# Optimization experiments

Measured on AMD Instinct MI355X. Metric: run time of the kernel, lower is better.

## Reference

```python
import jax, jax.numpy as jnp
import numpy as np

M, N, T = 4, 48, 256
H1 = (M + N) * 80          # 4160, linear1 out / GRU input
HID = M * M + N * N        # 2320, GRU hidden
H2 = M * N * 4             # 768
OUT = M * N                # 192


def _w(k, shape, fan_in):
    return jax.random.normal(k, shape, jnp.float32) / np.float32(np.sqrt(fan_in))


def setup_inputs() -> dict:
    key = jax.random.key(0)
    ks = jax.random.split(key, 12)
    A = (0.95 * jnp.eye(M, dtype=jnp.float32)
         + 0.05 * jax.random.normal(ks[0], (M, M), jnp.float32))  # stable dynamics
    return {
        "y_seq": jax.random.normal(ks[1], (N, T), jnp.float32),
        "x0": jax.random.normal(ks[2], (M,), jnp.float32),
        "h0": jax.random.normal(ks[3], (HID,), jnp.float32),  # self.hn (randn, zero_hidden_state=False)
        "A": A,
        "C": _w(ks[4], (N, M + 1), M + 1),
        "W1": _w(ks[5], (H1, M + N), M + N),
        "b1": jnp.zeros((H1,), jnp.float32),
        "W_ih": _w(ks[6], (3 * HID, H1), H1),
        "W_hh": _w(ks[7], (3 * HID, HID), HID),
        "b_ih": jnp.zeros((3 * HID,), jnp.float32),
        "b_hh": jnp.zeros((3 * HID,), jnp.float32),
        "W2": _w(ks[8], (H2, HID), HID),
        "b2": jnp.zeros((H2,), jnp.float32),
        "W3": _w(ks[9], (OUT, H2), H2),
        "b3": jnp.zeros((OUT,), jnp.float32),
    }


def _l2n(v):
    # torch F.normalize(p=2, eps=1e-12)
    return v / jnp.maximum(jnp.linalg.norm(v), 1e-12)


def reference(y_seq, x0, h0, A, C, W1, b1, W_ih, W_hh, b_ih, b_hh, W2, b2, W3, b3):
    m, n = A.shape[0], C.shape[0]
    one = jnp.ones((1,), A.dtype)

    def step(carry, y):
        x_post, h = carry
        x_prior = A @ x_post                                   # [m]
        y_prior = C @ jnp.concatenate([x_prior, one])           # [n]
        f2 = _l2n(y - y_prior)
        f4 = _l2n(x_post - x_prior)
        kg_in = jnp.concatenate([f2, f4])                       # [n+m]
        l1 = jax.nn.relu(W1 @ kg_in + b1)                       # [H1]
        # single GRU step (torch gate order: r, z, n)
        gi = W_ih @ l1 + b_ih
        gh = W_hh @ h + b_hh
        ir, iz, ig = jnp.split(gi, 3)
        hr, hz, hg = jnp.split(gh, 3)
        r = jax.nn.sigmoid(ir + hr)
        z = jax.nn.sigmoid(iz + hz)
        g = jnp.tanh(ig + r * hg)
        h_new = (1.0 - z) * g + z * h                           # [HID]
        l2 = jax.nn.relu(W2 @ h_new + b2)                       # [H2]
        kg = ((W3 @ l2 + b3) / 10000.0).reshape(m, n)           # Kalman gain
        x_new = x_prior + kg @ (y - y_prior)                    # posterior
        return (x_new, h_new), x_new

    _, xs = jax.lax.scan(step, (x0, h0), y_seq.T)               # xs: [T, m]
    return xs.T                                                 # [m, T]
```

## Files before the change

kernel.cpp:

```cpp
#include <hip/hip_runtime.h>
#include <hip/hip_cooperative_groups.h>

namespace cg = cooperative_groups;

#define T_STEPS 256

#define O_SLOT  0
#define O_EPOCH 1024
#define O_ZP    2048
#define O_HF    6144
#define HF_STR  9280
#define O_HB    24704
#define HB_STR  4672
#define O_GI    34048
#define O_GH    61888
#define O_PIH   90112
#define O_PHH   57997312
#define O_W2B   90514432
#define NEED_MIN 94077952
#define O_W1P   94077952
#define NEED_FULL 94543872

#define N_W2  1781760

#define WS_L1  0
#define WS_H0  4160
#define WS_H1  6480
#define WS_L2  8800
#define WS_V   9568
#define WS_C   12640

typedef __attribute__((ext_vector_type(8))) short bf16x8;
typedef __attribute__((ext_vector_type(4))) float f32x4;

__device__ __forceinline__ float wred(float v) {
#pragma unroll
  for (int m = 32; m; m >>= 1) v += __shfl_xor(v, m, 64);
  return v;
}
__device__ __forceinline__ float dot4(float4 a, float4 b) {
  return a.x * b.x + a.y * b.y + a.z * b.z + a.w * b.w;
}
__device__ __forceinline__ float blo(unsigned u) {
  unsigned t = u << 16; return __builtin_bit_cast(float, t);
}
__device__ __forceinline__ float bhi(unsigned u) {
  unsigned t = u & 0xFFFF0000u; return __builtin_bit_cast(float, t);
}
__device__ __forceinline__ float dot8bb(uint4 w, uint4 x) {
  float s;
  s  = blo(w.x) * blo(x.x) + bhi(w.x) * bhi(x.x);
  s += blo(w.y) * blo(x.y) + bhi(w.y) * bhi(x.y);
  s += blo(w.z) * blo(x.z) + bhi(w.z) * bhi(x.z);
  s += blo(w.w) * blo(x.w) + bhi(w.w) * bhi(x.w);
  return s;
}
__device__ __forceinline__ unsigned short f2bf(float f) {
  unsigned u = __builtin_bit_cast(unsigned, f);
  unsigned r = u + 0x7FFF + ((u >> 16) & 1);
  return (unsigned short)(r >> 16);
}

__device__ __forceinline__ void st_ag_f32(float* p, float v) {
  __hip_atomic_store(p, v, __ATOMIC_RELAXED, __HIP_MEMORY_SCOPE_AGENT);
}
__device__ __forceinline__ float ld_ag_f32(const float* p) {
  return __hip_atomic_load(p, __ATOMIC_RELAXED, __HIP_MEMORY_SCOPE_AGENT);
}
__device__ __forceinline__ void st_ag_u32(unsigned* p, unsigned v) {
  __hip_atomic_store(p, v, __ATOMIC_RELAXED, __HIP_MEMORY_SCOPE_AGENT);
}
__device__ __forceinline__ unsigned long long ld_ag_u64(const unsigned long long* p) {
  return __hip_atomic_load(p, __ATOMIC_RELAXED, __HIP_MEMORY_SCOPE_AGENT);
}

__device__ __forceinline__ void gbar(char* wsb, int bid, unsigned target, int* s_ok) {
  unsigned* slot  = (unsigned*)(wsb + O_SLOT);
  unsigned* epoch = (unsigned*)(wsb + O_EPOCH);
  const int tid = threadIdx.x;
  __syncthreads();
  if (bid == 0) {
    for (;;) {
      if (tid == 0) *s_ok = 1;
      __syncthreads();
      if (tid >= 1 && tid < 256) {
        if (__hip_atomic_load(&slot[tid], __ATOMIC_RELAXED, __HIP_MEMORY_SCOPE_AGENT) < target)
          *s_ok = 0;
      }
      __syncthreads();
      if (*s_ok) break;
      __builtin_amdgcn_s_sleep(2);
    }
    if (tid == 0)
      __hip_atomic_store(epoch, target, __ATOMIC_RELEASE, __HIP_MEMORY_SCOPE_AGENT);
    __syncthreads();
  } else {
    if (tid == 0) {
      __hip_atomic_store(&slot[bid], target, __ATOMIC_RELEASE, __HIP_MEMORY_SCOPE_AGENT);
      while (__hip_atomic_load(epoch, __ATOMIC_RELAXED, __HIP_MEMORY_SCOPE_AGENT) < target)
        __builtin_amdgcn_s_sleep(1);
    }
    __syncthreads();
  }
}

__global__ __launch_bounds__(256) void k_pack(const float* __restrict__ W,
                                              uint4* __restrict__ dst,
                                              int K, int NKT, int n) {
  int idx = blockIdx.x * 256 + threadIdx.x;
  int stride = gridDim.x * 256;
  for (; idx < n; idx += stride) {
    int l = idx & 63;
    int u = idx >> 6;
    int kt = u % NKT;
    int job = u / NKT;
    int g = job / 145, jt = job - g * 145;
    int row = g * 2320 + jt * 16 + (l & 15);
    int col = kt * 32 + ((l >> 4) << 3);
    const float* src = W + (size_t)row * K + col;
    unsigned short o[8];
    if (col + 7 < K) {
#pragma unroll
      for (int i = 0; i < 8; i++) o[i] = f2bf(src[i]);
    } else {
#pragma unroll
      for (int i = 0; i < 8; i++) o[i] = (col + i < K) ? f2bf(src[i]) : (unsigned short)0;
    }
    uint4 v;
    v.x = (unsigned)o[0] | ((unsigned)o[1] << 16);
    v.y = (unsigned)o[2] | ((unsigned)o[3] << 16);
    v.z = (unsigned)o[4] | ((unsigned)o[5] << 16);
    v.w = (unsigned)o[6] | ((unsigned)o[7] << 16);
    dst[idx] = v;
  }
}
__global__ __launch_bounds__(256) void k_cvt(const float4* __restrict__ src,
                                             ushort4* __restrict__ dst, int n4) {
  int i = blockIdx.x * 256 + threadIdx.x, st = gridDim.x * 256;
  for (; i < n4; i += st) {
    float4 v = src[i];
    ushort4 o;
    o.x = f2bf(v.x); o.y = f2bf(v.y); o.z = f2bf(v.z); o.w = f2bf(v.w);
    dst[i] = o;
  }
}
__global__ __launch_bounds__(256) void k_cvtw1(const float* __restrict__ W1,
                                               unsigned short* __restrict__ dst) {
  int i = blockIdx.x * 256 + threadIdx.x;
  if (i < 4160 * 56) {
    int r = i / 56, c = i - r * 56;
    dst[i] = (c < 52) ? f2bf(W1[r * 52 + c]) : (unsigned short)0;
  }
}
__global__ __launch_bounds__(256) void k_h0(const float* __restrict__ h0,
                                            unsigned short* __restrict__ hb0,
                                            unsigned short* __restrict__ hb1) {
  int j = blockIdx.x * 256 + threadIdx.x;
  if (j < 2336) {
    hb1[j] = (j < 2320) ? f2bf(h0[j]) : (unsigned short)0;
    if (j >= 2320) hb0[j] = 0;
  }
}

__global__ __launch_bounds__(1024, 4) void knet2(
    const float* __restrict__ y_seq, const float* __restrict__ x0,
    const float* __restrict__ h0, const float* __restrict__ A,
    const float* __restrict__ Cm, const float* __restrict__ W1,
    const float* __restrict__ b1, const float* __restrict__ b_ih,
    const float* __restrict__ b_hh, const float* __restrict__ b2,
    const float* __restrict__ W3, const float* __restrict__ b3,
    float* __restrict__ out, char* __restrict__ wsb, int use_w1p)
{
  const int tid  = threadIdx.x;
  const int lane = tid & 63;
  const int wav  = tid >> 6;
  const int bid  = blockIdx.x;

  float* zp  = (float*)(wsb + O_ZP);
  float* gi  = (float*)(wsb + O_GI);
  float* gh  = (float*)(wsb + O_GH);
  const unsigned short* bw2 = (const unsigned short*)(wsb + O_W2B);
  const uint4* w1p = (const uint4*)(wsb + O_W1P);

  __shared__ __align__(16) uint4 s_l1u[520];
  __shared__ __align__(16) uint4 s_h4u[292];
  __shared__ __align__(16) unsigned short s_h2[2336];
  __shared__ float s_part[4][4][16];
  __shared__ __align__(16) unsigned short s_kgb[64];
  __shared__ __align__(16) float s_kgf[52];
  __shared__ float s_innov[48];
  __shared__ float s_a[192];
  __shared__ float s_zred[384];
  __shared__ float s_l2loc[8];
  __shared__ float s_xpost[4], s_xprior[4], s_dx[4];
  __shared__ float s_sc2, s_sc4;
  __shared__ int s_ok;

  unsigned ep = 0;

  for (int t = 0; t <= T_STEPS; ++t) {
    if (t == 0) {
      if (tid < 4) s_xpost[tid] = x0[tid];
    } else {
      if (tid < 384) s_zred[tid] = ld_ag_f32(&zp[tid]);
      __syncthreads();
      if (tid < 4) {
        float z = 0.f;
#pragma unroll 8
        for (int p = 0; p < 96; ++p) z += s_zred[p * 4 + tid];
        float cb = 0.f;
        for (int j = 0; j < 48; ++j) cb += s_innov[j] * b3[tid * 48 + j];
        float xn = s_xprior[tid] + (z + cb) * 1e-4f;
        s_xpost[tid] = xn;
        if (bid == 0) out[tid * T_STEPS + (t - 1)] = xn;
      }
    }
    __syncthreads();
    if (t == T_STEPS) return;

    if (tid < 4) {
      float xpr = 0.f;
#pragma unroll
      for (int j = 0; j < 4; j++) xpr += A[tid * 4 + j] * s_xpost[j];
      s_xprior[tid] = xpr;
    }
    __syncthreads();
    if (tid < 48) {
      float yp = Cm[tid * 5 + 4];
#pragma unroll
      for (int j = 0; j < 4; j++) yp += Cm[tid * 5 + j] * s_xprior[j];
      s_innov[tid] = y_seq[tid * T_STEPS + t] - yp;
    }
    if (tid >= 64 && tid < 68) {
      int i = tid - 64;
      s_dx[i] = s_xpost[i] - s_xprior[i];
    }
    __syncthreads();
    if (tid == 0) {
      float s2 = 0.f;
      for (int r = 0; r < 48; r++) s2 += s_innov[r] * s_innov[r];
      s_sc2 = 1.0f / fmaxf(sqrtf(s2), 1e-12f);
      float s4 = 0.f;
      for (int i = 0; i < 4; i++) s4 += s_dx[i] * s_dx[i];
      s_sc4 = 1.0f / fmaxf(sqrtf(s4), 1e-12f);
    }
    __syncthreads();
    if (tid < 64) {
      float v = (tid < 48) ? s_innov[tid] * s_sc2
              : (tid < 52) ? s_dx[tid - 48] * s_sc4 : 0.f;
      s_kgb[tid] = f2bf(v);
      if (tid < 52) s_kgf[tid] = v;
    }
    {
      const unsigned long long* hbg =
          (const unsigned long long*)(wsb + O_HB + ((t + 1) & 1) * HB_STR);
      unsigned long long* dst = (unsigned long long*)s_h4u;
      if (tid < 584) dst[tid] = ld_ag_u64(hbg + tid);
    }
    __syncthreads();

    if (use_w1p) {
      const uint4* kg4 = (const uint4*)s_kgb;
      for (int r = tid; r < 4160; r += 1024) {
        const uint4* wr = w1p + (size_t)r * 7;
        float acc = b1[r];
#pragma unroll
        for (int c = 0; c < 7; c++) acc += dot8bb(wr[c], kg4[c]);
        ((unsigned short*)s_l1u)[r] = f2bf(fmaxf(acc, 0.f));
      }
    } else {
      const float4* kg4 = (const float4*)s_kgf;
      for (int r = tid; r < 4160; r += 1024) {
        const float4* wr = (const float4*)(W1 + (size_t)r * 52);
        float acc = b1[r];
#pragma unroll
        for (int c = 0; c < 13; c++) acc += dot4(wr[c], kg4[c]);
        ((unsigned short*)s_l1u)[r] = f2bf(fmaxf(acc, 0.f));
      }
    }
    __syncthreads();

    {
      const int q  = wav >> 2;
      const int kw = wav & 3;
      const int job = bid + 256 * q;
      if (job < 870) {
        const int side = (job < 435) ? 0 : 1;
        const int xoff = lane >> 4;
        const uint4* xs;
        const uint4* wp;
        int kbeg, kend;
        if (side == 0) {
          xs = s_l1u;
          kbeg = kw * 33; kend = kbeg + 33; if (kend > 130) kend = 130;
          wp = (const uint4*)(wsb + O_PIH) + ((size_t)job * 130 + kbeg) * 64 + lane;
        } else {
          xs = s_h4u;
          kbeg = kw * 19; kend = kbeg + 19; if (kend > 73) kend = 73;
          wp = (const uint4*)(wsb + O_PHH) + ((size_t)(job - 435) * 73 + kbeg) * 64 + lane;
        }
        f32x4 acc = {0.f, 0.f, 0.f, 0.f};
        uint4 b0  = wp[0 * 64];
        uint4 b1r = wp[1 * 64];
        uint4 b2r = wp[2 * 64];
        uint4 b3r = wp[3 * 64];
        uint4 b4  = wp[4 * 64];
        uint4 b5  = wp[5 * 64];
        uint4 b6  = wp[6 * 64];
        uint4 b7  = wp[7 * 64];
        int kt = kbeg;
#define GSTEP(P, B) { acc = __builtin_amdgcn_mfma_f32_16x16x32_bf16( \
            __builtin_bit_cast(bf16x8, B), \
            __builtin_bit_cast(bf16x8, xs[(kt + P) * 4 + xoff]), acc, 0, 0, 0); \
            B = wp[(size_t)(kt - kbeg + 8 + P) * 64]; }
        while (kt + 8 <= kend) {
          GSTEP(0, b0) GSTEP(1, b1r) GSTEP(2, b2r) GSTEP(3, b3r)
          GSTEP(4, b4) GSTEP(5, b5)  GSTEP(6, b6)  GSTEP(7, b7)
          kt += 8;
        }
#undef GSTEP
#define TSTEP(P, B) if (kt + P < kend) acc = __builtin_amdgcn_mfma_f32_16x16x32_bf16( \
            __builtin_bit_cast(bf16x8, B), \
            __builtin_bit_cast(bf16x8, xs[(kt + P) * 4 + xoff]), acc, 0, 0, 0);
        TSTEP(0, b0) TSTEP(1, b1r) TSTEP(2, b2r) TSTEP(3, b3r)
        TSTEP(4, b4) TSTEP(5, b5)  TSTEP(6, b6)  TSTEP(7, b7)
#undef TSTEP
        if ((lane & 15) == 0) {
          int rb = (lane >> 4) * 4;
#pragma unroll
          for (int i = 0; i < 4; i++) s_part[q][kw][rb + i] = acc[i];
        }
      }
    }
    __syncthreads();
    if (tid < 64) {
      int q = tid >> 4, r = tid & 15;
      int job = bid + 256 * q;
      if (job < 870) {
        float s = s_part[q][0][r] + s_part[q][1][r] + s_part[q][2][r] + s_part[q][3][r];
        if (job < 435) st_ag_f32(&gi[job * 16 + r], s);
        else st_ag_f32(&gh[(job - 435) * 16 + r], s);
      }
    }
    ++ep; gbar(wsb, bid, ep, &s_ok);

    if (bid < 96) {
      float* hf_out = (float*)(wsb + O_HF + (t & 1) * HF_STR);
      unsigned* hb_out32 = (unsigned*)(wsb + O_HB + (t & 1) * HB_STR);
      const float* hf_old = (const float*)(wsb + O_HF + ((t + 1) & 1) * HF_STR);
      for (int j = tid; j < 2320; j += 1024) {
        float ir = ld_ag_f32(&gi[j]) + b_ih[j];
        float iz = ld_ag_f32(&gi[2320 + j]) + b_ih[2320 + j];
        float ig = ld_ag_f32(&gi[4640 + j]) + b_ih[4640 + j];
        float hr = ld_ag_f32(&gh[j]) + b_hh[j];
        float hz = ld_ag_f32(&gh[2320 + j]) + b_hh[2320 + j];
        float hg = ld_ag_f32(&gh[4640 + j]) + b_hh[4640 + j];
        float rr = 1.f / (1.f + expf(-(ir + hr)));
        float zz = 1.f / (1.f + expf(-(iz + hz)));
        float gg = tanhf(ig + rr * hg);
        float hold = (t == 0) ? h0[j] : ld_ag_f32(&hf_old[j]);
        float hn = (1.f - zz) * gg + zz * hold;
        s_h2[j] = f2bf(hn);
        if (bid == 0) st_ag_f32(&hf_out[j], hn);
      }
      if (tid < 16) s_h2[2320 + tid] = 0;
      __syncthreads();
      if (bid == 0 && tid < 1168) {
        unsigned v = (unsigned)s_h2[2 * tid] | ((unsigned)s_h2[2 * tid + 1] << 16);
        st_ag_u32(hb_out32 + tid, v);
      }
      if (wav < 8) {
        const int row = bid * 8 + wav;
        const uint4* wr = (const uint4*)(bw2 + (size_t)row * 2320);
        const uint4* hx = (const uint4*)s_h2;
        float acc = 0.f;
        for (int k = lane; k < 290; k += 64) acc += dot8bb(wr[k], hx[k]);
        acc = wred(acc);
        if (lane == 0) s_l2loc[wav] = fmaxf(acc + b2[row], 0.f);
      }
      __syncthreads();
      if (tid < 192) {
        const float* w3r = W3 + (size_t)tid * 768 + bid * 8;
        float a = 0.f;
#pragma unroll
        for (int r = 0; r < 8; r++) a += w3r[r] * s_l2loc[r];
        s_a[tid] = a * s_innov[tid % 48];
      }
      __syncthreads();
      if (tid < 4) {
        float zv = 0.f;
        for (int j = 0; j < 48; j++) zv += s_a[tid * 48 + j];
        st_ag_f32(&zp[bid * 4 + tid], zv);
      }
    }
    ++ep; gbar(wsb, bid, ep, &s_ok);
  }
}

__global__ __launch_bounds__(256, 2) void knet(
    const float* __restrict__ y_seq, const float* __restrict__ x0,
    const float* __restrict__ h0, const float* __restrict__ A,
    const float* __restrict__ Cm, const float* __restrict__ W1,
    const float* __restrict__ b1, const float* __restrict__ W_ih,
    const float* __restrict__ W_hh, const float* __restrict__ b_ih,
    const float* __restrict__ b_hh, const float* __restrict__ W2,
    const float* __restrict__ b2, const float* __restrict__ W3,
    const float* __restrict__ b3, float* __restrict__ out,
    float* __restrict__ ws)
{
  cg::grid_group grid = cg::this_grid();
  const int tid = threadIdx.x, lane = tid & 63, wav = tid >> 6, bid = blockIdx.x;
  const int gt = bid * 256 + tid, wave_g = bid * 4 + wav, NW = gridDim.x * 4;

  __shared__ __align__(16) float4 s_buf4[1040];
  __shared__ __align__(16) float4 s_h4[580];
  __shared__ __align__(16) float s_kgin[52];
  __shared__ float s_innov[48];
  __shared__ float s_xpost[4], s_xprior[4], s_dx[4];
  __shared__ float s_sc2, s_sc4;

  for (int t = 0; t <= T_STEPS; ++t) {
    if (t == 0) {
      if (tid < 4) s_xpost[tid] = x0[tid];
    } else {
      const float4* vv  = (const float4*)(ws + WS_V + wav * 768);
      const float4* l2v = (const float4*)(ws + WS_L2);
      float acc = 0.f;
      for (int k = lane; k < 192; k += 64) acc += dot4(vv[k], l2v[k]);
      acc = wred(acc);
      if (lane == 0)
        s_xpost[wav] = s_xprior[wav] + (acc + ws[WS_C + wav]) * 1e-4f;
    }
    __syncthreads();
    if (bid == 0 && t > 0 && tid < 4) out[tid * T_STEPS + (t - 1)] = s_xpost[tid];
    if (t == T_STEPS) return;

    if (tid < 4) {
      float xp = 0.f;
#pragma unroll
      for (int j = 0; j < 4; j++) xp += A[tid * 4 + j] * s_xpost[j];
      s_xprior[tid] = xp;
    }
    __syncthreads();
    if (tid < 48) {
      float yp = Cm[tid * 5 + 4];
#pragma unroll
      for (int j = 0; j < 4; j++) yp += Cm[tid * 5 + j] * s_xprior[j];
      s_innov[tid] = y_seq[tid * T_STEPS + t] - yp;
    }
    if (tid >= 64 && tid < 68) {
      int i = tid - 64;
      s_dx[i] = s_xpost[i] - s_xprior[i];
    }
    __syncthreads();
    if (tid == 0) {
      float s2 = 0.f;
      for (int r = 0; r < 48; r++) s2 += s_innov[r] * s_innov[r];
      s_sc2 = 1.0f / fmaxf(sqrtf(s2), 1e-12f);
      float s4 = 0.f;
      for (int i = 0; i < 4; i++) s4 += s_dx[i] * s_dx[i];
      s_sc4 = 1.0f / fmaxf(sqrtf(s4), 1e-12f);
    }
    __syncthreads();
    if (tid < 48) s_kgin[tid] = s_innov[tid] * s_sc2;
    else if (tid < 52) s_kgin[tid] = s_dx[tid - 48] * s_sc4;
    __syncthreads();

    if (gt < 4160) {
      const float4* wr  = (const float4*)(W1 + (size_t)gt * 52);
      const float4* kg4 = (const float4*)s_kgin;
      float acc = b1[gt];
#pragma unroll
      for (int k = 0; k < 13; k++) acc += dot4(wr[k], kg4[k]);
      ws[WS_L1 + gt] = fmaxf(acc, 0.f);
    }
    grid.sync();

    {
      const float* h_old = (t == 0) ? h0 : (ws + (((t & 1) == 0) ? WS_H0 : WS_H1));
      float* h_new = ws + (((t & 1) == 0) ? WS_H1 : WS_H0);
      const float4* l1g = (const float4*)(ws + WS_L1);
      for (int i = tid; i < 1040; i += 256) s_buf4[i] = l1g[i];
      const float4* hog = (const float4*)h_old;
      for (int i = tid; i < 580; i += 256) s_h4[i] = hog[i];
      __syncthreads();
      const float* s_h = (const float*)s_h4;

      for (int j = wave_g; j < 2320; j += NW) {
        const float4* r0 = (const float4*)(W_ih + (size_t)j * 4160);
        const float4* r1 = (const float4*)(W_ih + (size_t)(j + 2320) * 4160);
        const float4* r2 = (const float4*)(W_ih + (size_t)(j + 4640) * 4160);
        float a0 = 0.f, a1 = 0.f, a2 = 0.f;
#pragma unroll 4
        for (int k = lane; k < 1040; k += 64) {
          float4 x = s_buf4[k];
          a0 += dot4(r0[k], x); a1 += dot4(r1[k], x); a2 += dot4(r2[k], x);
        }
        const float4* q0 = (const float4*)(W_hh + (size_t)j * 2320);
        const float4* q1 = (const float4*)(W_hh + (size_t)(j + 2320) * 2320);
        const float4* q2 = (const float4*)(W_hh + (size_t)(j + 4640) * 2320);
        float c0 = 0.f, c1 = 0.f, c2 = 0.f;
#pragma unroll 4
        for (int k = lane; k < 580; k += 64) {
          float4 x = s_h4[k];
          c0 += dot4(q0[k], x); c1 += dot4(q1[k], x); c2 += dot4(q2[k], x);
        }
        a0 = wred(a0); a1 = wred(a1); a2 = wred(a2);
        c0 = wred(c0); c1 = wred(c1); c2 = wred(c2);
        if (lane == 0) {
          float ir = a0 + b_ih[j], iz = a1 + b_ih[j + 2320], ig = a2 + b_ih[j + 4640];
          float hr = c0 + b_hh[j], hz = c1 + b_hh[j + 2320], hg = c2 + b_hh[j + 4640];
          float rr = 1.f / (1.f + expf(-(ir + hr)));
          float zz = 1.f / (1.f + expf(-(iz + hz)));
          float gg = tanhf(ig + rr * hg);
          h_new[j] = (1.f - zz) * gg + zz * s_h[j];
        }
      }
    }
    grid.sync();

    {
      const float* h_new = ws + (((t & 1) == 0) ? WS_H1 : WS_H0);
      const float4* hv = (const float4*)h_new;
      for (int i = tid; i < 580; i += 256) s_buf4[i] = hv[i];
      __syncthreads();

      if (gt < 3072) {
        int i = gt / 768, cc = gt - i * 768;
        const float* wcol = W3 + (size_t)(i * 48) * 768 + cc;
        float acc = 0.f;
#pragma unroll 8
        for (int j = 0; j < 48; j++) acc += s_innov[j] * wcol[(size_t)j * 768];
        ws[WS_V + gt] = acc;
      } else if (gt < 3076) {
        int i = gt - 3072;
        float acc = 0.f;
        for (int j = 0; j < 48; j++) acc += s_innov[j] * b3[i * 48 + j];
        ws[WS_C + i] = acc;
      }

      for (int task = wave_g; task < 768; task += NW) {
        const float4* row = (const float4*)(W2 + (size_t)task * 2320);
        float acc = 0.f;
#pragma unroll 4
        for (int k = lane; k < 580; k += 64) acc += dot4(row[k], s_buf4[k]);
        acc = wred(acc);
        if (lane == 0) ws[WS_L2 + task] = fmaxf(acc + b2[task], 0.f);
      }
    }
    grid.sync();
  }
}

extern "C" void kernel_launch(void* const* d_in, const int* in_sizes, int n_in,
                              void* d_out, int out_size, void* d_ws, size_t ws_size,
                              hipStream_t stream) {
  const float* y_seq = (const float*)d_in[0];
  const float* x0    = (const float*)d_in[1];
  const float* h0    = (const float*)d_in[2];
  const float* A     = (const float*)d_in[3];
  const float* Cm    = (const float*)d_in[4];
  const float* W1    = (const float*)d_in[5];
  const float* b1    = (const float*)d_in[6];
  const float* W_ih  = (const float*)d_in[7];
  const float* W_hh  = (const float*)d_in[8];
  const float* b_ih  = (const float*)d_in[9];
  const float* b_hh  = (const float*)d_in[10];
  const float* W2    = (const float*)d_in[11];
  const float* b2    = (const float*)d_in[12];
  const float* W3    = (const float*)d_in[13];
  const float* b3    = (const float*)d_in[14];
  float* out = (float*)d_out;
  float* ws  = (float*)d_ws;
  char* wsb  = (char*)d_ws;

  if (ws_size >= NEED_MIN) {
    int use_w1p = (ws_size >= NEED_FULL) ? 1 : 0;
    hipMemsetAsync(wsb + O_SLOT, 0, 2048, stream);
    k_pack<<<8192, 256, 0, stream>>>(W_ih, (uint4*)(wsb + O_PIH),
                                     4160, 130, 435 * 130 * 64);
    k_pack<<<8192, 256, 0, stream>>>(W_hh, (uint4*)(wsb + O_PHH),
                                     2320, 73, 435 * 73 * 64);
    k_cvt<<<512, 256, 0, stream>>>((const float4*)W2,
                                   (ushort4*)(wsb + O_W2B), N_W2 / 4);
    if (use_w1p)
      k_cvtw1<<<(4160 * 56 + 255) / 256, 256, 0, stream>>>(
          W1, (unsigned short*)(wsb + O_W1P));
    k_h0<<<10, 256, 0, stream>>>(h0, (unsigned short*)(wsb + O_HB),
                                 (unsigned short*)(wsb + O_HB + HB_STR));

    void* args[] = { &y_seq, &x0, &h0, &A, &Cm, &W1, &b1, &b_ih, &b_hh,
                     &b2, &W3, &b3, &out, &wsb, &use_w1p };
    hipError_t err = hipLaunchCooperativeKernel(
        reinterpret_cast<void*>(knet2), dim3(256), dim3(1024), args, 0, stream);
    if (err == hipSuccess) return;
  }

  {
    void* args[] = { &y_seq, &x0, &h0, &A, &Cm, &W1, &b1, &W_ih, &W_hh,
                     &b_ih, &b_hh, &W2, &b2, &W3, &b3, &out, &ws };
    hipLaunchCooperativeKernel(
        reinterpret_cast<void*>(knet), dim3(256), dim3(256), args, 0, stream);
  }
}
```

Baseline: 11.47 ms.

## Pin per-block W_ih slice in LDS and interleave gate outputs for vector loads

Each block now copies its q==0 slice of the packed W_ih weights (130x64 uint4, about 130KB) into dynamic LDS once before the time loop. The q==0 MFMA jobs then read weights from LDS on every step instead of streaming them from global memory, which removes a large share of the per-step HBM/L2 traffic. Gate pre-activations are also stored interleaved by gate (4 floats per row), so the GRU update can fetch them with 64-bit loads. The cost is a very large LDS allocation that could fail the cooperative launch or lower occupancy, in which case the code falls back to the slower kernel.

```diff
diff --git a/kernel.cpp b/kernel.cpp
--- a/kernel.cpp
+++ b/kernel.cpp
@@ -12,16 +12,18 @@
 #define HF_STR  9280
 #define O_HB    24704
 #define HB_STR  4672
-#define O_GI    34048
-#define O_GH    61888
-#define O_PIH   90112
-#define O_PHH   57997312
-#define O_W2B   90514432
-#define NEED_MIN 94077952
-#define O_W1P   94077952
-#define NEED_FULL 94543872
+#define O_GI4   34048
+#define O_GH4   71168
+#define O_PIH   108544
+#define O_PHH   58015744
+#define O_W2B   90532864
+#define NEED_MIN 94096384
+#define O_W1P   94096384
+#define NEED_FULL 94562304
 
 #define N_W2  1781760
+#define PIN_U4 (130 * 64)
+#define DYN_LDS 133120
 
 #define WS_L1  0
 #define WS_H0  4160
@@ -32,6 +34,7 @@
 
 typedef __attribute__((ext_vector_type(8))) short bf16x8;
 typedef __attribute__((ext_vector_type(4))) float f32x4;
+typedef unsigned long long u64t;
 
 __device__ __forceinline__ float wred(float v) {
 #pragma unroll
@@ -60,6 +63,14 @@
   unsigned r = u + 0x7FFF + ((u >> 16) & 1);
   return (unsigned short)(r >> 16);
 }
+__device__ __forceinline__ float u2f_lo(u64t v) {
+  unsigned u = (unsigned)(v & 0xFFFFFFFFull);
+  return __builtin_bit_cast(float, u);
+}
+__device__ __forceinline__ float u2f_hi(u64t v) {
+  unsigned u = (unsigned)(v >> 32);
+  return __builtin_bit_cast(float, u);
+}
 
 __device__ __forceinline__ void st_ag_f32(float* p, float v) {
   __hip_atomic_store(p, v, __ATOMIC_RELAXED, __HIP_MEMORY_SCOPE_AGENT);
@@ -70,7 +81,7 @@
 __device__ __forceinline__ void st_ag_u32(unsigned* p, unsigned v) {
   __hip_atomic_store(p, v, __ATOMIC_RELAXED, __HIP_MEMORY_SCOPE_AGENT);
 }
-__device__ __forceinline__ unsigned long long ld_ag_u64(const unsigned long long* p) {
+__device__ __forceinline__ u64t ld_ag_u64(const u64t* p) {
   return __hip_atomic_load(p, __ATOMIC_RELAXED, __HIP_MEMORY_SCOPE_AGENT);
 }
 
@@ -177,10 +188,13 @@
   const int bid  = blockIdx.x;
 
   float* zp  = (float*)(wsb + O_ZP);
-  float* gi  = (float*)(wsb + O_GI);
-  float* gh  = (float*)(wsb + O_GH);
+  float* gi4 = (float*)(wsb + O_GI4);
+  float* gh4 = (float*)(wsb + O_GH4);
   const unsigned short* bw2 = (const unsigned short*)(wsb + O_W2B);
   const uint4* w1p = (const uint4*)(wsb + O_W1P);
+
+  extern __shared__ __align__(16) char dynsmem[];
+  uint4* pin = (uint4*)dynsmem;
 
   __shared__ __align__(16) uint4 s_l1u[520];
   __shared__ __align__(16) uint4 s_h4u[292];
@@ -196,6 +210,11 @@
   __shared__ float s_sc2, s_sc4;
   __shared__ int s_ok;
 
+  {
+    const uint4* src = (const uint4*)(wsb + O_PIH) + (size_t)bid * PIN_U4;
+    for (int i = tid; i < PIN_U4; i += 1024) pin[i] = src[i];
+  }
+
   unsigned ep = 0;
 
   for (int t = 0; t <= T_STEPS; ++t) {
@@ -252,9 +271,8 @@
       if (tid < 52) s_kgf[tid] = v;
     }
     {
-      const unsigned long long* hbg =
-          (const unsigned long long*)(wsb + O_HB + ((t + 1) & 1) * HB_STR);
-      unsigned long long* dst = (unsigned long long*)s_h4u;
+      const u64t* hbg = (const u64t*)(wsb + O_HB + ((t + 1) & 1) * HB_STR);
+      u64t* dst = (u64t*)s_h4u;
       if (tid < 584) dst[tid] = ld_ag_u64(hbg + tid);
     }
     __syncthreads();
@@ -285,46 +303,55 @@
       const int kw = wav & 3;
       const int job = bid + 256 * q;
       if (job < 870) {
-        const int side = (job < 435) ? 0 : 1;
         const int xoff = lane >> 4;
-        const uint4* xs;
-        const uint4* wp;
-        int kbeg, kend;
-        if (side == 0) {
-          xs = s_l1u;
-          kbeg = kw * 33; kend = kbeg + 33; if (kend > 130) kend = 130;
-          wp = (const uint4*)(wsb + O_PIH) + ((size_t)job * 130 + kbeg) * 64 + lane;
+        f32x4 acc = {0.f, 0.f, 0.f, 0.f};
+        if (q == 0) {
+          int kbeg = kw * 33, kend = kbeg + 33; if (kend > 130) kend = 130;
+          const uint4* xs = s_l1u;
+          for (int kt = kbeg; kt < kend; ++kt)
+            acc = __builtin_amdgcn_mfma_f32_16x16x32_bf16(
+                __builtin_bit_cast(bf16x8, pin[kt * 64 + lane]),
+                __builtin_bit_cast(bf16x8, xs[kt * 4 + xoff]), acc, 0, 0, 0);
         } else {
-          xs = s_h4u;
-          kbeg = kw * 19; kend = kbeg + 19; if (kend > 73) kend = 73;
-          wp = (const uint4*)(wsb + O_PHH) + ((size_t)(job - 435) * 73 + kbeg) * 64 + lane;
-        }
-        f32x4 acc = {0.f, 0.f, 0.f, 0.f};
-        uint4 b0  = wp[0 * 64];
-        uint4 b1r = wp[1 * 64];
-        uint4 b2r = wp[2 * 64];
-        uint4 b3r = wp[3 * 64];
-        uint4 b4  = wp[4 * 64];
-        uint4 b5  = wp[5 * 64];
-        uint4 b6  = wp[6 * 64];
-        uint4 b7  = wp[7 * 64];
-        int kt = kbeg;
+          const int side = (job < 435) ? 0 : 1;
+          const uint4* xs;
+          const uint4* wp;
+          int kbeg, kend;
+          if (side == 0) {
+            xs = s_l1u;
+            kbeg = kw * 33; kend = kbeg + 33; if (kend > 130) kend = 130;
+            wp = (const uint4*)(wsb + O_PIH) + ((size_t)job * 130 + kbeg) * 64 + lane;
+          } else {
+            xs = s_h4u;
+            kbeg = kw * 19; kend = kbeg + 19; if (kend > 73) kend = 73;
+            wp = (const uint4*)(wsb + O_PHH) + ((size_t)(job - 435) * 73 + kbeg) * 64 + lane;
+          }
+          uint4 b0  = wp[0 * 64];
+          uint4 b1r = wp[1 * 64];
+          uint4 b2r = wp[2 * 64];
+          uint4 b3r = wp[3 * 64];
+          uint4 b4  = wp[4 * 64];
+          uint4 b5  = wp[5 * 64];
+          uint4 b6  = wp[6 * 64];
+          uint4 b7  = wp[7 * 64];
+          int kt = kbeg;
 #define GSTEP(P, B) { acc = __builtin_amdgcn_mfma_f32_16x16x32_bf16( \
-            __builtin_bit_cast(bf16x8, B), \
-            __builtin_bit_cast(bf16x8, xs[(kt + P) * 4 + xoff]), acc, 0, 0, 0); \
-            B = wp[(size_t)(kt - kbeg + 8 + P) * 64]; }
-        while (kt + 8 <= kend) {
-          GSTEP(0, b0) GSTEP(1, b1r) GSTEP(2, b2r) GSTEP(3, b3r)
-          GSTEP(4, b4) GSTEP(5, b5)  GSTEP(6, b6)  GSTEP(7, b7)
-          kt += 8;
-        }
+              __builtin_bit_cast(bf16x8, B), \
+              __builtin_bit_cast(bf16x8, xs[(kt + P) * 4 + xoff]), acc, 0, 0, 0); \
+              B = wp[(size_t)(kt - kbeg + 8 + P) * 64]; }
+          while (kt + 8 <= kend) {
+            GSTEP(0, b0) GSTEP(1, b1r) GSTEP(2, b2r) GSTEP(3, b3r)
+            GSTEP(4, b4) GSTEP(5, b5)  GSTEP(6, b6)  GSTEP(7, b7)
+            kt += 8;
+          }
 #undef GSTEP
 #define TSTEP(P, B) if (kt + P < kend) acc = __builtin_amdgcn_mfma_f32_16x16x32_bf16( \
-            __builtin_bit_cast(bf16x8, B), \
-            __builtin_bit_cast(bf16x8, xs[(kt + P) * 4 + xoff]), acc, 0, 0, 0);
-        TSTEP(0, b0) TSTEP(1, b1r) TSTEP(2, b2r) TSTEP(3, b3r)
-        TSTEP(4, b4) TSTEP(5, b5)  TSTEP(6, b6)  TSTEP(7, b7)
+              __builtin_bit_cast(bf16x8, B), \
+              __builtin_bit_cast(bf16x8, xs[(kt + P) * 4 + xoff]), acc, 0, 0, 0);
+          TSTEP(0, b0) TSTEP(1, b1r) TSTEP(2, b2r) TSTEP(3, b3r)
+          TSTEP(4, b4) TSTEP(5, b5)  TSTEP(6, b6)  TSTEP(7, b7)
 #undef TSTEP
+        }
         if ((lane & 15) == 0) {
           int rb = (lane >> 4) * 4;
 #pragma unroll
@@ -338,8 +365,14 @@
       int job = bid + 256 * q;
       if (job < 870) {
         float s = s_part[q][0][r] + s_part[q][1][r] + s_part[q][2][r] + s_part[q][3][r];
-        if (job < 435) st_ag_f32(&gi[job * 16 + r], s);
-        else st_ag_f32(&gh[(job - 435) * 16 + r], s);
+        if (job < 435) {
+          int g = job / 145, jt = job - g * 145;
+          st_ag_f32(&gi4[(size_t)(jt * 16 + r) * 4 + g], s);
+        } else {
+          int j2 = job - 435;
+          int g = j2 / 145, jt = j2 - g * 145;
+          st_ag_f32(&gh4[(size_t)(jt * 16 + r) * 4 + g], s);
+        }
       }
     }
     ++ep; gbar(wsb, bid, ep, &s_ok);
@@ -348,13 +381,19 @@
       float* hf_out = (float*)(wsb + O_HF + (t & 1) * HF_STR);
       unsigned* hb_out32 = (unsigned*)(wsb + O_HB + (t & 1) * HB_STR);
       const float* hf_old = (const float*)(wsb + O_HF + ((t + 1) & 1) * HF_STR);
+      const u64t* gi2 = (const u64t*)gi4;
+      const u64t* gh2 = (const u64t*)gh4;
       for (int j = tid; j < 2320; j += 1024) {
-        float ir = ld_ag_f32(&gi[j]) + b_ih[j];
-        float iz = ld_ag_f32(&gi[2320 + j]) + b_ih[2320 + j];
-        float ig = ld_ag_f32(&gi[4640 + j]) + b_ih[4640 + j];
-        float hr = ld_ag_f32(&gh[j]) + b_hh[j];
-        float hz = ld_ag_f32(&gh[2320 + j]) + b_hh[2320 + j];
-        float hg = ld_ag_f32(&gh[4640 + j]) + b_hh[4640 + j];
+        u64t ia = ld_ag_u64(&gi2[(size_t)j * 2]);
+        u64t ib = ld_ag_u64(&gi2[(size_t)j * 2 + 1]);
+        u64t ha = ld_ag_u64(&gh2[(size_t)j * 2]);
+        u64t hb = ld_ag_u64(&gh2[(size_t)j * 2 + 1]);
+        float ir = u2f_lo(ia) + b_ih[j];
+        float iz = u2f_hi(ia) + b_ih[2320 + j];
+        float ig = u2f_lo(ib) + b_ih[4640 + j];
+        float hr = u2f_lo(ha) + b_hh[j];
+        float hz = u2f_hi(ha) + b_hh[2320 + j];
+        float hg = u2f_lo(hb) + b_hh[4640 + j];
         float rr = 1.f / (1.f + expf(-(ir + hr)));
         float zz = 1.f / (1.f + expf(-(iz + hz)));
         float gg = tanhf(ig + rr * hg);
@@ -576,6 +615,8 @@
 
   if (ws_size >= NEED_MIN) {
     int use_w1p = (ws_size >= NEED_FULL) ? 1 : 0;
+    hipFuncSetAttribute(reinterpret_cast<const void*>(knet2),
+                        hipFuncAttributeMaxDynamicSharedMemorySize, DYN_LDS + 2048);
     hipMemsetAsync(wsb + O_SLOT, 0, 2048, stream);
     k_pack<<<8192, 256, 0, stream>>>(W_ih, (uint4*)(wsb + O_PIH),
                                      4160, 130, 435 * 130 * 64);
@@ -592,7 +633,7 @@
     void* args[] = { &y_seq, &x0, &h0, &A, &Cm, &W1, &b1, &b_ih, &b_hh,
                      &b2, &W3, &b3, &out, &wsb, &use_w1p };
     hipError_t err = hipLaunchCooperativeKernel(
-        reinterpret_cast<void*>(knet2), dim3(256), dim3(1024), args, 0, stream);
+        reinterpret_cast<void*>(knet2), dim3(256), dim3(1024), args, DYN_LDS, stream);
     if (err == hipSuccess) return;
   }
 
```

Result: faster. 10.72 ms (-6.5%).
